# Optimization experiments

Measured on AMD Instinct MI355X. Metric: run time of the kernel, lower is better.

Reference implementation:

```python
import jax, jax.numpy as jnp
import numpy as np
from functools import partial

N_NODES = 100000
N_EDGES = 1600000
N_LABEL = 200000
D = 128


def _add_self_loops(edge_index, edge_weight, num_nodes):
    # PyG GCNConv default: add self loops with fill_value = 1.0
    loops = jnp.arange(num_nodes, dtype=edge_index.dtype)
    src = jnp.concatenate([edge_index[0], loops])
    dst = jnp.concatenate([edge_index[1], loops])
    ew = jnp.concatenate([edge_weight, jnp.ones((num_nodes,), edge_weight.dtype)])
    return src, dst, ew


def _gcn_norm(src, dst, ew, num_nodes):
    # symmetric normalization: D^-1/2 A D^-1/2, degrees over target index
    deg = jax.ops.segment_sum(ew, dst, num_segments=num_nodes)
    dinv = jnp.where(deg > 0, jax.lax.rsqrt(deg), 0.0)
    return dinv[src] * ew * dinv[dst]


def _gcn_conv(x, W, b, src, dst, norm, num_nodes):
    h = x @ W                      # [N, D] small GEMM
    msg = h[src] * norm[:, None]   # gather + scale, [E+N, D]
    out = jax.ops.segment_sum(msg, dst, num_segments=num_nodes)
    return out + b


def setup_inputs() -> dict:
    key = jax.random.key(0)
    ks = jax.random.split(key, 10)
    s = 1.0 / np.sqrt(D)
    return {
        "x": jax.random.normal(ks[0], (N_NODES, D), jnp.float32),
        "edge_index": jax.random.randint(ks[1], (2, N_EDGES), 0, N_NODES, jnp.int64),
        "edge_weight": jax.random.uniform(ks[2], (N_EDGES,), jnp.float32),
        "edge_label_index": jax.random.randint(ks[3], (2, N_LABEL), 0, N_NODES, jnp.int64),
        "W1": jax.random.uniform(ks[4], (D, D), jnp.float32, -s, s),
        "b1": jnp.zeros((D,), jnp.float32),
        "W2": jax.random.uniform(ks[5], (D, D), jnp.float32, -s, s),
        "b2": jnp.zeros((D,), jnp.float32),
        "lin_W": jax.random.uniform(ks[6], (D, D), jnp.float32, -s, s),
        "lin_b": jax.random.uniform(ks[7], (D,), jnp.float32, -s, s),
    }


def reference(x, edge_index, edge_weight, edge_label_index, W1, b1, W2, b2, lin_W, lin_b):
    n = x.shape[0]
    src, dst, ew = _add_self_loops(edge_index, edge_weight, n)
    norm = _gcn_norm(src, dst, ew, n)
    out = jax.nn.relu(_gcn_conv(x, W1, b1, src, dst, norm, n))
    out = jax.nn.relu(_gcn_conv(out, W2, b2, src, dst, norm, n))
    had = out[edge_label_index[0]] * out[edge_label_index[1]]  # [EL, D]
    # lin then sum over features == had @ lin_W @ 1 + sum(lin_b)
    return jnp.sum(had @ lin_W + lin_b, axis=-1)
```

## Files before the change

kernel.cpp:

```cpp
#include <hip/hip_runtime.h>

#define N_NODES 100000
#define N_EDGES 1600000
#define N_LABEL 200000
#define D 128

#define SCAN_BLOCKS ((N_NODES + 255) / 256)

typedef __attribute__((ext_vector_type(8))) short short8;
typedef __attribute__((ext_vector_type(4))) float f32x4;

static __device__ __forceinline__ unsigned short f2bf(float f) {
    unsigned u = __float_as_uint(f);
    u += 0x7fffu + ((u >> 16) & 1u);
    return (unsigned short)(u >> 16);
}
static __device__ __forceinline__ float bf2f_lo(unsigned p) {
    return __uint_as_float(p << 16);
}
static __device__ __forceinline__ float bf2f_hi(unsigned p) {
    return __uint_as_float(p & 0xffff0000u);
}

__global__ void k_prepall(const float* __restrict__ linW, const float* __restrict__ linb,
                          const float* __restrict__ W1, const float* __restrict__ W2,
                          float* __restrict__ wv, float* __restrict__ cval,
                          unsigned short* __restrict__ w1t,
                          unsigned short* __restrict__ w2t,
                          int* __restrict__ cnt8) {
    int b = blockIdx.x;
    if (b == 0) {
        int t = threadIdx.x;
        if (t < 128) {
            float s = 0.f;
            for (int j = 0; j < D; ++j) s += linW[t * D + j];
            wv[t] = s;
        }
        __shared__ float red[128];
        if (t < 128) red[t] = linb[t];
        __syncthreads();
        for (int st = 64; st > 0; st >>= 1) {
            if (t < st) red[t] += red[t + st];
            __syncthreads();
        }
        if (t == 0) *cval = red[0];
    } else if (b <= 64) {
        int i = (b - 1) * 256 + threadIdx.x;
        int k = i >> 7, n = i & 127;
        w1t[n * D + k] = f2bf(W1[i]);
    } else if (b <= 128) {
        int i = (b - 65) * 256 + threadIdx.x;
        int k = i >> 7, n = i & 127;
        w2t[n * D + k] = f2bf(W2[i]);
    } else {
        int i = (b - 129) * 256 + threadIdx.x;
        if (i < 8 * N_NODES) cnt8[i] = 0;
    }
}

__global__ void k_count(const int* __restrict__ ei, int* __restrict__ cnt8,
                        int* __restrict__ rank) {
    int e = blockIdx.x * 256 + threadIdx.x;
    int p = blockIdx.x & 7;
    if (e < N_EDGES) rank[e] = atomicAdd(&cnt8[p * N_NODES + ei[N_EDGES + e]], 1);
}

__global__ void k_scan1(const int* __restrict__ cnt8, int* __restrict__ offs,
                        int* __restrict__ bsum) {
    __shared__ int sm[256];
    int tid = threadIdx.x;
    int i = blockIdx.x * 256 + tid;
    int v = 0;
    if (i < N_NODES) {
#pragma unroll
        for (int q = 0; q < 8; ++q) v += cnt8[q * N_NODES + i];
    }
    sm[tid] = v;
    __syncthreads();
    for (int st = 1; st < 256; st <<= 1) {
        int add = (tid >= st) ? sm[tid - st] : 0;
        __syncthreads();
        sm[tid] += add;
        __syncthreads();
    }
    if (i < N_NODES) offs[i] = sm[tid] - v;
    if (tid == 255) bsum[blockIdx.x] = sm[255];
}

__global__ void k_scan3(int* __restrict__ offs, const int* __restrict__ bsum,
                        const int* __restrict__ cnt8, int* __restrict__ pofs) {
    __shared__ int preSm;
    int tid = threadIdx.x;
    if (tid < 64) {
        int s = 0;
        for (int j = tid; j < (int)blockIdx.x; j += 64) s += bsum[j];
#pragma unroll
        for (int st = 32; st > 0; st >>= 1) s += __shfl_down(s, st, 64);
        if (tid == 0) preSm = s;
    }
    __syncthreads();
    int pre = preSm;
    int i = blockIdx.x * 256 + tid;
    if (i < N_NODES) {
        int base = offs[i] + pre;
        offs[i] = base;
#pragma unroll
        for (int q = 0; q < 8; ++q) {
            pofs[q * N_NODES + i] = base;
            base += cnt8[q * N_NODES + i];
        }
    }
    if (i == 0) offs[N_NODES] = N_EDGES;
}

__global__ void k_scatter(const int* __restrict__ ei, const float* __restrict__ ew,
                          const int* __restrict__ pofs, const int* __restrict__ rank,
                          int2* __restrict__ csr) {
    int e = blockIdx.x * 256 + threadIdx.x;
    int p = blockIdx.x & 7;
    if (e < N_EDGES) {
        int d = ei[N_EDGES + e];
        int pos = pofs[p * N_NODES + d] + rank[e];
        csr[pos] = make_int2(ei[e] << 6, __float_as_int(ew[e]));
    }
}

__global__ void k_degdinv(const int* __restrict__ offs, const int2* __restrict__ csr,
                          float* __restrict__ dinv) {
    int i = blockIdx.x * 256 + threadIdx.x;
    if (i < N_NODES) {
        int p0 = offs[i], p1 = offs[i + 1];
        float s = 1.0f;
        for (int p = p0; p < p1; ++p) s += __int_as_float(csr[p].y);
        dinv[i] = rsqrtf(s);
    }
}

template <bool IN_F32>
__global__ __launch_bounds__(256) void k_gemm(const void* __restrict__ INp,
                                              const unsigned short* __restrict__ Wt,
                                              const float* __restrict__ dinv,
                                              unsigned short* __restrict__ H) {
    __shared__ unsigned short xs[64 * 128];
    __shared__ unsigned short wts[128 * 128];
    int tid = threadIdx.x;
    int rowBase = blockIdx.x * 64;

#pragma unroll
    for (int i = 0; i < 4; ++i) {
        int idx = tid + i * 256;
        int r = idx >> 4;
        int kc = (idx & 15) << 3;
        int gr = rowBase + r;
        uint4 pk = make_uint4(0, 0, 0, 0);
        if (gr < N_NODES) {
            if (IN_F32) {
                const float* X = (const float*)INp;
                float4 v0 = *(const float4*)&X[(size_t)gr * D + kc];
                float4 v1 = *(const float4*)&X[(size_t)gr * D + kc + 4];
                pk.x = (unsigned)f2bf(v0.x) | ((unsigned)f2bf(v0.y) << 16);
                pk.y = (unsigned)f2bf(v0.z) | ((unsigned)f2bf(v0.w) << 16);
                pk.z = (unsigned)f2bf(v1.x) | ((unsigned)f2bf(v1.y) << 16);
                pk.w = (unsigned)f2bf(v1.z) | ((unsigned)f2bf(v1.w) << 16);
            } else {
                pk = *(const uint4*)&((const unsigned short*)INp)[(size_t)gr * D + kc];
            }
        }
        *(uint4*)&xs[(r * D + kc) ^ ((r & 7) << 3)] = pk;
    }
#pragma unroll
    for (int i = 0; i < 8; ++i) {
        int idx = tid + i * 256;
        int n = idx >> 4;
        int kc = (idx & 15) << 3;
        uint4 pk = *(const uint4*)&Wt[n * D + kc];
        *(uint4*)&wts[(n * D + kc) ^ ((n & 7) << 3)] = pk;
    }
    __syncthreads();

    int lane = tid & 63;
    int wrow = (tid >> 6) * 16;
    int l15 = lane & 15;
    int l4 = (lane >> 4) << 2;

    f32x4 acc[8] = {};
    union FragU { short8 v; uint2 u2[2]; };

#pragma unroll
    for (int kk = 0; kk < 4; ++kk) {
        int kb = kk * 32 + l4;
        int m = wrow + l15;
        FragU a;
        a.u2[0] = *(uint2*)&xs[(m * D + kb) ^ ((m & 7) << 3)];
        a.u2[1] = *(uint2*)&xs[(m * D + kb + 16) ^ ((m & 7) << 3)];
#pragma unroll
        for (int ct = 0; ct < 8; ++ct) {
            int n = ct * 16 + l15;
            FragU b;
            b.u2[0] = *(uint2*)&wts[(n * D + kb) ^ ((n & 7) << 3)];
            b.u2[1] = *(uint2*)&wts[(n * D + kb + 16) ^ ((n & 7) << 3)];
            acc[ct] = __builtin_amdgcn_mfma_f32_16x16x32_bf16(a.v, b.v, acc[ct], 0, 0, 0);
        }
    }

    int rloc = wrow + l4;
    float dn[4];
#pragma unroll
    for (int r = 0; r < 4; ++r) {
        int gr = rowBase + rloc + r;
        dn[r] = (gr < N_NODES) ? dinv[gr] : 0.f;
    }
#pragma unroll
    for (int ct = 0; ct < 8; ++ct) {
#pragma unroll
        for (int r = 0; r < 4; ++r) {
            int gr = rowBase + rloc + r;
            if (gr < N_NODES)
                H[(size_t)gr * D + ct * 16 + l15] = f2bf(acc[ct][r] * dn[r]);
        }
    }
}

__global__ __launch_bounds__(256) void k_agg(const unsigned* __restrict__ h,
                                             const float* __restrict__ dinv,
                                             const int* __restrict__ offs,
                                             const int2* __restrict__ csr,
                                             const float* __restrict__ bias,
                                             unsigned* __restrict__ out) {
    int lane = threadIdx.x & 63;
    int node = __builtin_amdgcn_readfirstlane(blockIdx.x * 4 + (threadIdx.x >> 6));
    if (node >= N_NODES) return;

    int p0 = offs[node], p1 = offs[node + 1];
    float a0 = 0.f, a1 = 0.f;

    for (int p = p0; p < p1; p += 8) {
        int2 cc[8];
        float ww[8];
#pragma unroll
        for (int k = 0; k < 8; ++k) {
            int pe = p + k;
            bool v = pe < p1;
            cc[k] = csr[v ? pe : p0];
            ww[k] = v ? __int_as_float(cc[k].y) : 0.f;
        }
        unsigned hh[8];
#pragma unroll
        for (int k = 0; k < 8; ++k)
            hh[k] = h[(size_t)(unsigned)cc[k].x + lane];
#pragma unroll
        for (int k = 0; k < 8; ++k) {
            a0 += ww[k] * bf2f_lo(hh[k]);
            a1 += ww[k] * bf2f_hi(hh[k]);
        }
    }

    unsigned sv = h[(size_t)node * 64 + lane];
    a0 += bf2f_lo(sv);
    a1 += bf2f_hi(sv);
    float dn = dinv[node];
    float2 bb = *(const float2*)&bias[lane * 2];
    a0 = fmaxf(a0 * dn + bb.x, 0.f);
    a1 = fmaxf(a1 * dn + bb.y, 0.f);
    out[(size_t)node * 64 + lane] = (unsigned)f2bf(a0) | ((unsigned)f2bf(a1) << 16);
}

__global__ void k_final(const int* __restrict__ eli, const unsigned* __restrict__ o2,
                        const float* __restrict__ wv, const float* __restrict__ cval,
                        float* __restrict__ res) {
    unsigned g = blockIdx.x * 256 + threadIdx.x;
    int l = g >> 5;
    int t = g & 31;
    if (l < N_LABEL) {
        int a = eli[l];
        int b = eli[N_LABEL + l];
        uint2 ua = *(const uint2*)&o2[(size_t)a * 64 + t * 2];
        uint2 ub = *(const uint2*)&o2[(size_t)b * 64 + t * 2];
        float4 w4 = *(const float4*)&wv[t * 4];
        float s = bf2f_lo(ua.x) * bf2f_lo(ub.x) * w4.x
                + bf2f_hi(ua.x) * bf2f_hi(ub.x) * w4.y
                + bf2f_lo(ua.y) * bf2f_lo(ub.y) * w4.z
                + bf2f_hi(ua.y) * bf2f_hi(ub.y) * w4.w;
#pragma unroll
        for (int st = 16; st > 0; st >>= 1) s += __shfl_down(s, st, 32);
        if (t == 0) res[l] = s + *cval;
    }
}

extern "C" void kernel_launch(void* const* d_in, const int* in_sizes, int n_in,
                              void* d_out, int out_size, void* d_ws, size_t ws_size,
                              hipStream_t stream) {
    const float* x    = (const float*)d_in[0];
    const int*   ei   = (const int*)d_in[1];
    const float* ew   = (const float*)d_in[2];
    const int*   eli  = (const int*)d_in[3];
    const float* W1   = (const float*)d_in[4];
    const float* b1   = (const float*)d_in[5];
    const float* W2   = (const float*)d_in[6];
    const float* b2   = (const float*)d_in[7];
    const float* linW = (const float*)d_in[8];
    const float* linb = (const float*)d_in[9];
    float* res = (float*)d_out;

    float*          ws    = (float*)d_ws;
    float*          dinv  = ws;
    int*            offs  = (int*)(dinv + N_NODES);
    int*            bsum  = offs + N_NODES + 4;
    int*            cnt8  = bsum + 512;
    int*            pofs  = cnt8 + 8 * N_NODES;
    int2*           csr   = (int2*)(pofs + 8 * N_NODES);
    unsigned*       h_bf  = (unsigned*)(csr + N_EDGES);
    unsigned*       agg   = h_bf + (size_t)N_NODES * 64;
    unsigned*       out2  = agg + (size_t)N_NODES * 64;
    float*          wv    = (float*)(out2 + (size_t)N_NODES * 64);
    float*          cval  = wv + D;
    unsigned short* w1t   = (unsigned short*)(cval + 1);
    unsigned short* w2t   = w1t + D * D;
    int*            rank  = (int*)agg;

    k_prepall<<<129 + (8 * N_NODES + 255) / 256, 256, 0, stream>>>(
        linW, linb, W1, W2, wv, cval, w1t, w2t, cnt8);

    k_count<<<(N_EDGES + 255) / 256, 256, 0, stream>>>(ei, cnt8, rank);
    k_scan1<<<SCAN_BLOCKS, 256, 0, stream>>>(cnt8, offs, bsum);
    k_scan3<<<SCAN_BLOCKS, 256, 0, stream>>>(offs, bsum, cnt8, pofs);
    k_scatter<<<(N_EDGES + 255) / 256, 256, 0, stream>>>(ei, ew, pofs, rank, csr);
    k_degdinv<<<(N_NODES + 255) / 256, 256, 0, stream>>>(offs, csr, dinv);

    const int GB = (N_NODES + 63) / 64;

    k_gemm<true><<<GB, 256, 0, stream>>>(x, w1t, dinv, (unsigned short*)h_bf);
    k_agg<<<(N_NODES + 3) / 4, 256, 0, stream>>>(h_bf, dinv, offs, csr, b1, agg);

    k_gemm<false><<<GB, 256, 0, stream>>>(agg, w2t, dinv, (unsigned short*)h_bf);
    k_agg<<<(N_NODES + 3) / 4, 256, 0, stream>>>(h_bf, dinv, offs, csr, b2, out2);

    k_final<<<(N_LABEL * 32 + 255) / 256, 256, 0, stream>>>(eli, out2, wv, cval, res);
}
```

Measured before the change: 352.3 us.

## Fuse degree computation into first GEMM and first aggregation into second GEMM

Drops the separate degree/dinv kernel and computes it wave-cooperatively inside the first GEMM, writing dinv and scaling rows from shared memory. Fuses the first-layer aggregation (bias, ReLU, bf16 pack) with the second GEMM so the aggregated features stay in LDS instead of going through global memory. This removes two launches and one full N×D write and read. The cost is that each block aggregates only 64 nodes, one wave per 16 nodes serially, before its MFMA stage, and W2 fragments are read straight from global memory rather than staged in LDS.

```diff
diff --git a/kernel.cpp b/kernel.cpp
--- a/kernel.cpp
+++ b/kernel.cpp
@@ -125,26 +125,35 @@
     }
 }
 
-__global__ void k_degdinv(const int* __restrict__ offs, const int2* __restrict__ csr,
-                          float* __restrict__ dinv) {
-    int i = blockIdx.x * 256 + threadIdx.x;
-    if (i < N_NODES) {
-        int p0 = offs[i], p1 = offs[i + 1];
-        float s = 1.0f;
-        for (int p = p0; p < p1; ++p) s += __int_as_float(csr[p].y);
-        dinv[i] = rsqrtf(s);
-    }
-}
-
-template <bool IN_F32>
-__global__ __launch_bounds__(256) void k_gemm(const void* __restrict__ INp,
-                                              const unsigned short* __restrict__ Wt,
-                                              const float* __restrict__ dinv,
-                                              unsigned short* __restrict__ H) {
+__global__ __launch_bounds__(256) void k_gemm1d(const float* __restrict__ X,
+                                                const unsigned short* __restrict__ Wt,
+                                                const int* __restrict__ offs,
+                                                const int2* __restrict__ csr,
+                                                float* __restrict__ dinv,
+                                                unsigned short* __restrict__ H) {
     __shared__ unsigned short xs[64 * 128];
     __shared__ unsigned short wts[128 * 128];
+    __shared__ float dsm[64];
     int tid = threadIdx.x;
+    int lane = tid & 63;
     int rowBase = blockIdx.x * 64;
+    int w = __builtin_amdgcn_readfirstlane(tid >> 6);
+
+    for (int t = 0; t < 16; ++t) {
+        int node = rowBase + w * 16 + t;
+        float dv = 0.f;
+        if (node < N_NODES) {
+            int p0 = offs[node], p1 = offs[node + 1];
+            float s = 0.f;
+            for (int pp = p0 + lane; pp < p1; pp += 64)
+                s += __int_as_float(csr[pp].y);
+#pragma unroll
+            for (int st = 32; st > 0; st >>= 1) s += __shfl_xor(s, st, 64);
+            dv = rsqrtf(1.0f + s);
+            if (lane == 0) dinv[node] = dv;
+        }
+        if (lane == 0) dsm[w * 16 + t] = dv;
+    }
 
 #pragma unroll
     for (int i = 0; i < 4; ++i) {
@@ -154,17 +163,12 @@
         int gr = rowBase + r;
         uint4 pk = make_uint4(0, 0, 0, 0);
         if (gr < N_NODES) {
-            if (IN_F32) {
-                const float* X = (const float*)INp;
-                float4 v0 = *(const float4*)&X[(size_t)gr * D + kc];
-                float4 v1 = *(const float4*)&X[(size_t)gr * D + kc + 4];
-                pk.x = (unsigned)f2bf(v0.x) | ((unsigned)f2bf(v0.y) << 16);
-                pk.y = (unsigned)f2bf(v0.z) | ((unsigned)f2bf(v0.w) << 16);
-                pk.z = (unsigned)f2bf(v1.x) | ((unsigned)f2bf(v1.y) << 16);
-                pk.w = (unsigned)f2bf(v1.z) | ((unsigned)f2bf(v1.w) << 16);
-            } else {
-                pk = *(const uint4*)&((const unsigned short*)INp)[(size_t)gr * D + kc];
-            }
+            float4 v0 = *(const float4*)&X[(size_t)gr * D + kc];
+            float4 v1 = *(const float4*)&X[(size_t)gr * D + kc + 4];
+            pk.x = (unsigned)f2bf(v0.x) | ((unsigned)f2bf(v0.y) << 16);
+            pk.y = (unsigned)f2bf(v0.z) | ((unsigned)f2bf(v0.w) << 16);
+            pk.z = (unsigned)f2bf(v1.x) | ((unsigned)f2bf(v1.y) << 16);
+            pk.w = (unsigned)f2bf(v1.z) | ((unsigned)f2bf(v1.w) << 16);
         }
         *(uint4*)&xs[(r * D + kc) ^ ((r & 7) << 3)] = pk;
     }
@@ -178,8 +182,7 @@
     }
     __syncthreads();
 
-    int lane = tid & 63;
-    int wrow = (tid >> 6) * 16;
+    int wrow = w * 16;
     int l15 = lane & 15;
     int l4 = (lane >> 4) << 2;
 
@@ -199,6 +202,97 @@
             FragU b;
             b.u2[0] = *(uint2*)&wts[(n * D + kb) ^ ((n & 7) << 3)];
             b.u2[1] = *(uint2*)&wts[(n * D + kb + 16) ^ ((n & 7) << 3)];
+            acc[ct] = __builtin_amdgcn_mfma_f32_16x16x32_bf16(a.v, b.v, acc[ct], 0, 0, 0);
+        }
+    }
+
+    int rloc = wrow + l4;
+    float dn[4];
+#pragma unroll
+    for (int r = 0; r < 4; ++r) dn[r] = dsm[rloc + r];
+#pragma unroll
+    for (int ct = 0; ct < 8; ++ct) {
+#pragma unroll
+        for (int r = 0; r < 4; ++r) {
+            int gr = rowBase + rloc + r;
+            if (gr < N_NODES)
+                H[(size_t)gr * D + ct * 16 + l15] = f2bf(acc[ct][r] * dn[r]);
+        }
+    }
+}
+
+__global__ __launch_bounds__(256) void k_agg_gemm(const unsigned* __restrict__ h,
+                                                  const float* __restrict__ dinv,
+                                                  const int* __restrict__ offs,
+                                                  const int2* __restrict__ csr,
+                                                  const float* __restrict__ bias,
+                                                  const unsigned short* __restrict__ Wt,
+                                                  unsigned short* __restrict__ H) {
+    __shared__ unsigned short xs[64 * 128];
+    int tid = threadIdx.x;
+    int lane = tid & 63;
+    int rowBase = blockIdx.x * 64;
+    int w = __builtin_amdgcn_readfirstlane(tid >> 6);
+
+    float2 bb = *(const float2*)&bias[lane * 2];
+    for (int t = 0; t < 16; ++t) {
+        int nodeLoc = w * 16 + t;
+        int node = rowBase + nodeLoc;
+        unsigned val = 0;
+        if (node < N_NODES) {
+            int p0 = offs[node], p1 = offs[node + 1];
+            float a0 = 0.f, a1 = 0.f;
+            for (int p = p0; p < p1; p += 8) {
+                int2 cc[8];
+                float ww[8];
+#pragma unroll
+                for (int k = 0; k < 8; ++k) {
+                    int pe = p + k;
+                    bool v = pe < p1;
+                    cc[k] = csr[v ? pe : p0];
+                    ww[k] = v ? __int_as_float(cc[k].y) : 0.f;
+                }
+                unsigned hh[8];
+#pragma unroll
+                for (int k = 0; k < 8; ++k)
+                    hh[k] = h[(size_t)(unsigned)cc[k].x + lane];
+#pragma unroll
+                for (int k = 0; k < 8; ++k) {
+                    a0 += ww[k] * bf2f_lo(hh[k]);
+                    a1 += ww[k] * bf2f_hi(hh[k]);
+                }
+            }
+            unsigned sv = h[(size_t)node * 64 + lane];
+            a0 += bf2f_lo(sv);
+            a1 += bf2f_hi(sv);
+            float dnn = dinv[node];
+            a0 = fmaxf(a0 * dnn + bb.x, 0.f);
+            a1 = fmaxf(a1 * dnn + bb.y, 0.f);
+            val = (unsigned)f2bf(a0) | ((unsigned)f2bf(a1) << 16);
+        }
+        *(unsigned*)&xs[((nodeLoc * D) + (lane << 1)) ^ ((nodeLoc & 7) << 3)] = val;
+    }
+
+    int wrow = w * 16;
+    int l15 = lane & 15;
+    int l4 = (lane >> 4) << 2;
+
+    f32x4 acc[8] = {};
+    union FragU { short8 v; uint2 u2[2]; };
+
+#pragma unroll
+    for (int kk = 0; kk < 4; ++kk) {
+        int kb = kk * 32 + l4;
+        int m = wrow + l15;
+        FragU a;
+        a.u2[0] = *(uint2*)&xs[(m * D + kb) ^ ((m & 7) << 3)];
+        a.u2[1] = *(uint2*)&xs[(m * D + kb + 16) ^ ((m & 7) << 3)];
+#pragma unroll
+        for (int ct = 0; ct < 8; ++ct) {
+            int n = ct * 16 + l15;
+            FragU b;
+            b.u2[0] = *(const uint2*)&Wt[n * D + kb];
+            b.u2[1] = *(const uint2*)&Wt[n * D + kb + 16];
             acc[ct] = __builtin_amdgcn_mfma_f32_16x16x32_bf16(a.v, b.v, acc[ct], 0, 0, 0);
         }
     }
@@ -310,13 +404,13 @@
     int*            pofs  = cnt8 + 8 * N_NODES;
     int2*           csr   = (int2*)(pofs + 8 * N_NODES);
     unsigned*       h_bf  = (unsigned*)(csr + N_EDGES);
-    unsigned*       agg   = h_bf + (size_t)N_NODES * 64;
-    unsigned*       out2  = agg + (size_t)N_NODES * 64;
+    unsigned*       h2    = h_bf + (size_t)N_NODES * 64;
+    unsigned*       out2  = h2 + (size_t)N_NODES * 64;
     float*          wv    = (float*)(out2 + (size_t)N_NODES * 64);
     float*          cval  = wv + D;
     unsigned short* w1t   = (unsigned short*)(cval + 1);
     unsigned short* w2t   = w1t + D * D;
-    int*            rank  = (int*)agg;
+    int*            rank  = (int*)h2;
 
     k_prepall<<<129 + (8 * N_NODES + 255) / 256, 256, 0, stream>>>(
         linW, linb, W1, W2, wv, cval, w1t, w2t, cnt8);
@@ -325,15 +419,15 @@
     k_scan1<<<SCAN_BLOCKS, 256, 0, stream>>>(cnt8, offs, bsum);
     k_scan3<<<SCAN_BLOCKS, 256, 0, stream>>>(offs, bsum, cnt8, pofs);
     k_scatter<<<(N_EDGES + 255) / 256, 256, 0, stream>>>(ei, ew, pofs, rank, csr);
-    k_degdinv<<<(N_NODES + 255) / 256, 256, 0, stream>>>(offs, csr, dinv);
 
     const int GB = (N_NODES + 63) / 64;
 
-    k_gemm<true><<<GB, 256, 0, stream>>>(x, w1t, dinv, (unsigned short*)h_bf);
-    k_agg<<<(N_NODES + 3) / 4, 256, 0, stream>>>(h_bf, dinv, offs, csr, b1, agg);
-
-    k_gemm<false><<<GB, 256, 0, stream>>>(agg, w2t, dinv, (unsigned short*)h_bf);
-    k_agg<<<(N_NODES + 3) / 4, 256, 0, stream>>>(h_bf, dinv, offs, csr, b2, out2);
+    k_gemm1d<<<GB, 256, 0, stream>>>(x, w1t, offs, csr, dinv, (unsigned short*)h_bf);
+
+    k_agg_gemm<<<GB, 256, 0, stream>>>(h_bf, dinv, offs, csr, b1, w2t,
+                                       (unsigned short*)h2);
+
+    k_agg<<<(N_NODES + 3) / 4, 256, 0, stream>>>(h2, dinv, offs, csr, b2, out2);
 
     k_final<<<(N_LABEL * 32 + 255) / 256, 256, 0, stream>>>(eli, out2, wv, cval, res);
 }
```

New measurement: 402.2 us. +14.2%, slower.
